# Optimization experiments

Measured on AMD Instinct MI355X. Metric: run time of the kernel, lower is better.

## Reference

```python
import jax, jax.numpy as jnp
import numpy as np
import math

H = 768      # hidden_size
NH = 12      # num_head
DH = H // NH # head dim
FF = 4 * H
EPS = 1e-6

def _layernorm(x, g, b):
    mu = jnp.mean(x, axis=-1, keepdims=True)
    var = jnp.mean(jnp.square(x - mu), axis=-1, keepdims=True)
    return (x - mu) * jax.lax.rsqrt(var + EPS) * g + b

def setup_inputs() -> dict:
    key = jax.random.key(0)
    ks = jax.random.split(key, 16)
    B, N = 8, 1024
    xav = lambda k, i, o: jax.random.uniform(k, (i, o), jnp.float32, -1.0, 1.0) * math.sqrt(6.0 / (i + o))
    bias = lambda k, o: jax.random.normal(k, (o,), jnp.float32) * 1e-6
    return {
        "x": jax.random.normal(ks[0], (B, N, H), jnp.float32),
        "wq": xav(ks[1], H, H), "bq": bias(ks[2], H),
        "wk": xav(ks[3], H, H), "bk": bias(ks[4], H),
        "wv": xav(ks[5], H, H), "bv": bias(ks[6], H),
        "wo": xav(ks[7], H, H), "bo": bias(ks[8], H),
        "w1": xav(ks[9], H, FF), "b1": bias(ks[10], FF),
        "w2": xav(ks[11], FF, H), "b2": bias(ks[12], H),
        "g1": jnp.ones((H,), jnp.float32), "be1": jnp.zeros((H,), jnp.float32),
        "g2": jnp.ones((H,), jnp.float32), "be2": jnp.zeros((H,), jnp.float32),
    }

def reference(x, wq, bq, wk, bk, wv, bv, wo, bo, w1, b1, w2, b2, g1, be1, g2, be2):
    B, N, _ = x.shape
    x1 = _layernorm(x, g1, be1)
    # QKV projections -> (B, NH, N, DH)
    split = lambda t: t.reshape(B, N, NH, DH).transpose(0, 2, 1, 3)
    q = split(x1 @ wq + bq)
    k = split(x1 @ wk + bk)
    v = split(x1 @ wv + bv)
    # NOTE: original divides by sqrt(attention_size)=sqrt(H), not sqrt(DH)
    scores = jnp.einsum("bhqd,bhkd->bhqk", q, k) / math.sqrt(H)
    weights = jax.nn.softmax(scores, axis=-1)
    ctx = jnp.einsum("bhqk,bhkd->bhqd", weights, v)
    ctx = ctx.transpose(0, 2, 1, 3).reshape(B, N, H)
    attn_out = ctx @ wo + bo  # dropout is identity in eval
    x = x + attn_out
    x2 = _layernorm(x, g2, be2)
    h = jax.nn.gelu(x2 @ w1 + b1, approximate=False)  # torch F.gelu is exact erf gelu
    mlp_out = h @ w2 + b2
    x = x + mlp_out
    return (x, weights)
```

## Files before the change

kernel.cpp:

```cpp
#include <hip/hip_runtime.h>
#include <cstdint>
#include <cstddef>

#define H 768
#define NHEAD 12
#define DH 64
#define FFD 3072
#define BATCH 8
#define SEQ 1024
#define NTOK (BATCH*SEQ)
#define QKVS 2304

typedef __bf16 bf16x8 __attribute__((ext_vector_type(8)));
typedef float  floatx4 __attribute__((ext_vector_type(4)));

#define MFMA_BF16(a,b,c) __builtin_amdgcn_mfma_f32_16x16x32_bf16((a),(b),(c),0,0,0)

__device__ __forceinline__ void gload16(const void* g, void* l) {
    __builtin_amdgcn_global_load_lds((const __attribute__((address_space(1))) void*)g,
                                     (__attribute__((address_space(3))) void*)l,
                                     16, 0, 0);
}

__global__ __launch_bounds__(256) void ln_kernel(const float* __restrict__ x,
                                                 const float* __restrict__ g,
                                                 const float* __restrict__ be,
                                                 __bf16* __restrict__ out) {
    int row  = blockIdx.x * 4 + (threadIdx.x >> 6);
    int lane = threadIdx.x & 63;
    const float* xr = x + (size_t)row * H;
    float v[12];
    float s = 0.f;
#pragma unroll
    for (int i = 0; i < 12; i++) { v[i] = xr[lane + i * 64]; s += v[i]; }
#pragma unroll
    for (int m = 32; m >= 1; m >>= 1) s += __shfl_xor(s, m, 64);
    float mu = s * (1.0f / H);
    float q = 0.f;
#pragma unroll
    for (int i = 0; i < 12; i++) { float d = v[i] - mu; q += d * d; }
#pragma unroll
    for (int m = 32; m >= 1; m >>= 1) q += __shfl_xor(q, m, 64);
    float rstd = rsqrtf(q * (1.0f / H) + 1e-6f);
    __bf16* orow = out + (size_t)row * H;
#pragma unroll
    for (int i = 0; i < 12; i++) {
        int c = lane + i * 64;
        orow[c] = (__bf16)((v[i] - mu) * rstd * g[c] + be[c]);
    }
}

__global__ __launch_bounds__(256) void wtrans_kernel(const float* __restrict__ W,
                                                     __bf16* __restrict__ T,
                                                     int K, int Nn) {
    __shared__ float tile[32][33];
    int tx = threadIdx.x & 31;
    int ty = threadIdx.x >> 5;
    int n0 = blockIdx.x * 32, k0 = blockIdx.y * 32;
#pragma unroll
    for (int i = 0; i < 32; i += 8)
        tile[ty + i][tx] = W[(size_t)(k0 + ty + i) * Nn + n0 + tx];
    __syncthreads();
#pragma unroll
    for (int i = 0; i < 32; i += 8)
        T[(size_t)(n0 + ty + i) * K + k0 + tx] = (__bf16)tile[tx][ty + i];
}

__global__ __launch_bounds__(256) void bcat_kernel(const float* __restrict__ bq,
                                                   const float* __restrict__ bk,
                                                   const float* __restrict__ bv,
                                                   float* __restrict__ o) {
    int i = blockIdx.x * 256 + threadIdx.x;
    if (i >= 3 * H) return;
    if (i < H) o[i] = bq[i];
    else if (i < 2 * H) o[i] = bk[i - H];
    else o[i] = bv[i - 2 * H];
}

__global__ __launch_bounds__(256) void vtrans_kernel(const __bf16* __restrict__ qkv,
                                                     __bf16* __restrict__ vT) {
    __shared__ __bf16 tile[64][65];
    int b = blockIdx.z, h = blockIdx.y, n0 = blockIdx.x * 64;
    int tx = threadIdx.x, ty = threadIdx.y;
#pragma unroll
    for (int r = ty; r < 64; r += 4)
        tile[r][tx] = qkv[((size_t)b * SEQ + n0 + r) * QKVS + 2 * H + h * DH + tx];
    __syncthreads();
#pragma unroll
    for (int c = ty; c < 64; c += 4)
        vT[(((size_t)b * NHEAD + h) * DH + c) * SEQ + n0 + tx] = tile[tx][c];
}

template<bool GELU, bool HAS_RES, bool OUT_BF16>
__global__ __launch_bounds__(256) void gemm_kernel(const __bf16* __restrict__ A,
                                                   const __bf16* __restrict__ Bt,
                                                   const float* __restrict__ bias,
                                                   const float* __restrict__ res,
                                                   __bf16* __restrict__ obf,
                                                   float* __restrict__ ofp,
                                                   int Nn, int K) {
    __shared__ __bf16 As[128 * 32];
    __shared__ __bf16 Bs[128 * 32];
    int tid = threadIdx.x;
    int wave = tid >> 6, lane = tid & 63;
    int wr = wave >> 1, wc = wave & 1;
    int l15 = lane & 15, quad = lane >> 4;

    floatx4 acc[4][4];
    floatx4 zero = {0.f, 0.f, 0.f, 0.f};
#pragma unroll
    for (int i = 0; i < 4; i++)
#pragma unroll
        for (int j = 0; j < 4; j++) acc[i][j] = zero;

    int c0 = wave * 2, c1 = c0 + 1;
    int lr = lane >> 2, lc = (lane & 3) * 8;
    const __bf16* Ag0 = A + (size_t)(blockIdx.y * 128 + c0 * 16 + lr) * K + lc;
    const __bf16* Ag1 = A + (size_t)(blockIdx.y * 128 + c1 * 16 + lr) * K + lc;
    const __bf16* Bg0 = Bt + (size_t)(blockIdx.x * 128 + c0 * 16 + lr) * K + lc;
    const __bf16* Bg1 = Bt + (size_t)(blockIdx.x * 128 + c1 * 16 + lr) * K + lc;
    __bf16* AsD0 = &As[c0 * 512];
    __bf16* AsD1 = &As[c1 * 512];
    __bf16* BsD0 = &Bs[c0 * 512];
    __bf16* BsD1 = &Bs[c1 * 512];

    for (int k0 = 0; k0 < K; k0 += 32) {
        gload16(Ag0 + k0, AsD0);
        gload16(Ag1 + k0, AsD1);
        gload16(Bg0 + k0, BsD0);
        gload16(Bg1 + k0, BsD1);
        __syncthreads();
        bf16x8 af[4], bfv[4];
#pragma unroll
        for (int i = 0; i < 4; i++)
            af[i] = *(const bf16x8*)&As[(wr * 64 + i * 16 + l15) * 32 + quad * 8];
#pragma unroll
        for (int j = 0; j < 4; j++)
            bfv[j] = *(const bf16x8*)&Bs[(wc * 64 + j * 16 + l15) * 32 + quad * 8];
#pragma unroll
        for (int i = 0; i < 4; i++)
#pragma unroll
            for (int j = 0; j < 4; j++)
                acc[i][j] = MFMA_BF16(af[i], bfv[j], acc[i][j]);
        __syncthreads();
    }

#pragma unroll
    for (int i = 0; i < 4; i++) {
        int row = blockIdx.y * 128 + wr * 64 + i * 16 + quad * 4;
#pragma unroll
        for (int j = 0; j < 4; j++) {
            int col = blockIdx.x * 128 + wc * 64 + j * 16 + l15;
            float bsv = bias[col];
#pragma unroll
            for (int r = 0; r < 4; r++) {
                float vv = acc[i][j][r] + bsv;
                if (GELU) vv = 0.5f * vv * (1.0f + erff(vv * 0.70710678118654752f));
                if (HAS_RES) vv += res[(size_t)(row + r) * Nn + col];
                if (OUT_BF16) obf[(size_t)(row + r) * Nn + col] = (__bf16)vv;
                else          ofp[(size_t)(row + r) * Nn + col] = vv;
            }
        }
    }
}

__device__ __forceinline__ int sbidx(int row, int col) {
    return row * 1024 + (col ^ ((row & 7) << 3));
}

__global__ __launch_bounds__(256, 4) void attn_kernel(const __bf16* __restrict__ qkv,
                                                      const __bf16* __restrict__ vT,
                                                      float* __restrict__ Wout,
                                                      __bf16* __restrict__ ctx) {
    __shared__ __bf16 Sb[16 * 1024];
    __shared__ __align__(16) float red[2][16][4];
    int tid = threadIdx.x;
    int wave = tid >> 6, lane = tid & 63, l15 = lane & 15, quad = lane >> 4;
    int rt = blockIdx.x, h = blockIdx.y, b = blockIdx.z;
    const size_t tokbase = (size_t)b * SEQ * QKVS + h * DH;
    const float scale = 0.03608439182435161f;

    const __bf16* qrow = qkv + tokbase + (size_t)(rt * 16 + l15) * QKVS;
    bf16x8 qf0 = *(const bf16x8*)(qrow + quad * 8);
    bf16x8 qf1 = *(const bf16x8*)(qrow + 32 + quad * 8);

    floatx4 s[16];
    const __bf16* kbase = qkv + tokbase + H;
#pragma unroll
    for (int i = 0; i < 16; i++) {
        int ct = wave * 16 + i;
        const __bf16* krow = kbase + (size_t)(ct * 16 + l15) * QKVS;
        bf16x8 kf0 = *(const bf16x8*)(krow + quad * 8);
        bf16x8 kf1 = *(const bf16x8*)(krow + 32 + quad * 8);
        floatx4 a = {0.f, 0.f, 0.f, 0.f};
        a = MFMA_BF16(qf0, kf0, a);
        a = MFMA_BF16(qf1, kf1, a);
#pragma unroll
        for (int r = 0; r < 4; r++) s[i][r] = a[r] * scale;
    }

    float m4[4];
#pragma unroll
    for (int r = 0; r < 4; r++) {
        float m = s[0][r];
#pragma unroll
        for (int i = 1; i < 16; i++) m = fmaxf(m, s[i][r]);
#pragma unroll
        for (int msk = 8; msk >= 1; msk >>= 1) m = fmaxf(m, __shfl_xor(m, msk, 64));
        m4[r] = m;
    }
    if (l15 == 0) {
#pragma unroll
        for (int r = 0; r < 4; r++) red[0][quad * 4 + r][wave] = m4[r];
    }
    __syncthreads();
    float mrow[4];
#pragma unroll
    for (int r = 0; r < 4; r++) {
        float4 rr = *(const float4*)&red[0][quad * 4 + r][0];
        mrow[r] = fmaxf(fmaxf(rr.x, rr.y), fmaxf(rr.z, rr.w));
    }

    float s4[4] = {0.f, 0.f, 0.f, 0.f};
#pragma unroll
    for (int i = 0; i < 16; i++) {
#pragma unroll
        for (int r = 0; r < 4; r++) {
            float e = __expf(s[i][r] - mrow[r]);
            s[i][r] = e;
            s4[r] += e;
        }
    }
#pragma unroll
    for (int r = 0; r < 4; r++) {
#pragma unroll
        for (int msk = 8; msk >= 1; msk >>= 1) s4[r] += __shfl_xor(s4[r], msk, 64);
    }
    if (l15 == 0) {
#pragma unroll
        for (int r = 0; r < 4; r++) red[1][quad * 4 + r][wave] = s4[r];
    }
    __syncthreads();
    float inv[4];
#pragma unroll
    for (int r = 0; r < 4; r++) {
        float4 rr = *(const float4*)&red[1][quad * 4 + r][0];
        inv[r] = 1.0f / (rr.x + rr.y + rr.z + rr.w);
    }

    size_t wbase = (((size_t)b * NHEAD + h) * SEQ + rt * 16) * SEQ;
#pragma unroll
    for (int i = 0; i < 16; i++) {
        int col = (wave * 16 + i) * 16 + l15;
#pragma unroll
        for (int r = 0; r < 4; r++) {
            float w = s[i][r] * inv[r];
            int row = quad * 4 + r;
            __builtin_nontemporal_store(w, &Wout[wbase + (size_t)row * SEQ + col]);
            Sb[sbidx(row, col)] = (__bf16)w;
        }
    }
    __syncthreads();

    floatx4 acc = {0.f, 0.f, 0.f, 0.f};
    const __bf16* vbase = vT + (((size_t)b * NHEAD + h) * DH + wave * 16 + l15) * SEQ;
#pragma unroll
    for (int c = 0; c < 32; c++) {
        int k0 = c * 32 + quad * 8;
        bf16x8 af = *(const bf16x8*)&Sb[sbidx(l15, k0)];
        bf16x8 bv = *(const bf16x8*)(vbase + k0);
        acc = MFMA_BF16(af, bv, acc);
    }
#pragma unroll
    for (int r = 0; r < 4; r++)
        ctx[((size_t)b * SEQ + rt * 16 + quad * 4 + r) * H + h * DH + wave * 16 + l15] =
            (__bf16)acc[r];
}

extern "C" void kernel_launch(void* const* d_in, const int* in_sizes, int n_in,
                              void* d_out, int out_size, void* d_ws, size_t ws_size,
                              hipStream_t stream) {
    const float* x   = (const float*)d_in[0];
    const float* wq  = (const float*)d_in[1];
    const float* bq  = (const float*)d_in[2];
    const float* wk  = (const float*)d_in[3];
    const float* bk  = (const float*)d_in[4];
    const float* wv  = (const float*)d_in[5];
    const float* bv  = (const float*)d_in[6];
    const float* wo  = (const float*)d_in[7];
    const float* bo  = (const float*)d_in[8];
    const float* w1  = (const float*)d_in[9];
    const float* b1  = (const float*)d_in[10];
    const float* w2  = (const float*)d_in[11];
    const float* b2  = (const float*)d_in[12];
    const float* g1  = (const float*)d_in[13];
    const float* be1 = (const float*)d_in[14];
    const float* g2  = (const float*)d_in[15];
    const float* be2 = (const float*)d_in[16];

    char* ws = (char*)d_ws;
    const size_t SZB = (size_t)NTOK * H * 2;
    __bf16* x1b  = (__bf16*)(ws);
    __bf16* qkvb = (__bf16*)(ws + SZB);
    __bf16* vTb  = (__bf16*)(ws + 4 * SZB);
    __bf16* ctxb = (__bf16*)(ws + 5 * SZB);
    __bf16* x2b  = (__bf16*)(ws + 6 * SZB);
    __bf16* hb   = (__bf16*)(ws + 7 * SZB);
    size_t off = 7 * SZB + (size_t)NTOK * FFD * 2;
    float* xattn = (float*)(ws + off); off += (size_t)NTOK * H * 4;
    __bf16* wqkvT = (__bf16*)(ws + off); off += (size_t)3 * H * H * 2;
    __bf16* woT  = (__bf16*)(ws + off); off += (size_t)H * H * 2;
    __bf16* w1T  = (__bf16*)(ws + off); off += (size_t)H * FFD * 2;
    __bf16* w2T  = (__bf16*)(ws + off); off += (size_t)FFD * H * 2;
    float* bqkv  = (float*)(ws + off); off += (size_t)3 * H * 4;

    float* outx = (float*)d_out;
    float* outw = (float*)d_out + (size_t)NTOK * H;

    wtrans_kernel<<<dim3(24, 24), 256, 0, stream>>>(wq, wqkvT, H, H);
    wtrans_kernel<<<dim3(24, 24), 256, 0, stream>>>(wk, wqkvT + (size_t)H * H, H, H);
    wtrans_kernel<<<dim3(24, 24), 256, 0, stream>>>(wv, wqkvT + (size_t)2 * H * H, H, H);
    wtrans_kernel<<<dim3(24, 24), 256, 0, stream>>>(wo, woT, H, H);
    wtrans_kernel<<<dim3(96, 24), 256, 0, stream>>>(w1, w1T, H, FFD);
    wtrans_kernel<<<dim3(24, 96), 256, 0, stream>>>(w2, w2T, FFD, H);
    bcat_kernel<<<9, 256, 0, stream>>>(bq, bk, bv, bqkv);

    ln_kernel<<<NTOK / 4, 256, 0, stream>>>(x, g1, be1, x1b);

    gemm_kernel<false, false, true><<<dim3(QKVS / 128, NTOK / 128), 256, 0, stream>>>(
        x1b, wqkvT, bqkv, nullptr, qkvb, nullptr, QKVS, H);

    vtrans_kernel<<<dim3(16, NHEAD, BATCH), dim3(64, 4), 0, stream>>>(qkvb, vTb);

    attn_kernel<<<dim3(64, NHEAD, BATCH), 256, 0, stream>>>(qkvb, vTb, outw, ctxb);

    gemm_kernel<false, true, false><<<dim3(H / 128, NTOK / 128), 256, 0, stream>>>(
        ctxb, woT, bo, x, nullptr, xattn, H, H);

    ln_kernel<<<NTOK / 4, 256, 0, stream>>>(xattn, g2, be2, x2b);

    gemm_kernel<true, false, true><<<dim3(FFD / 128, NTOK / 128), 256, 0, stream>>>(
        x2b, w1T, b1, nullptr, hb, nullptr, FFD, H);

    gemm_kernel<false, true, false><<<dim3(H / 128, NTOK / 128), 256, 0, stream>>>(
        hb, w2T, b2, xattn, nullptr, outx, H, FFD);
}
```

Before: 864.6 us.

## Merge prep kernels, use fast GELU erf approximation, remap attention blocks per XCD

Combines the six weight-transpose launches, the bias concat and the first layernorm into a single prep kernel, cutting seven kernel launches. Replaces erff in the GELU epilogue with an Abramowitz-Stegun polynomial built on a fast reciprocal and exponential, reducing epilogue ALU cost at some loss of accuracy. Remaps attention block indices so that all row tiles of a (batch, head) pair land on the same XCD, aiming to improve K/V reuse in that XCD's L2.

After: 851.3 us. No clear change (-1.5%).

```diff
diff --git a/kernel.cpp b/kernel.cpp
--- a/kernel.cpp
+++ b/kernel.cpp
@@ -20,6 +20,91 @@
     __builtin_amdgcn_global_load_lds((const __attribute__((address_space(1))) void*)g,
                                      (__attribute__((address_space(3))) void*)l,
                                      16, 0, 0);
+}
+
+__device__ __forceinline__ float gelu_erf(float x) {
+    float z = fabsf(x) * 0.70710678118654752f;
+    float t = __builtin_amdgcn_rcpf(1.0f + 0.3275911f * z);
+    float poly = t * (0.254829592f +
+               t * (-0.284496736f +
+               t * (1.421413741f +
+               t * (-1.453152027f +
+               t * 1.061405429f))));
+    float e = __expf(-z * z);
+    float erfv = 1.0f - poly * e;
+    erfv = copysignf(erfv, x);
+    return 0.5f * x * (1.0f + erfv);
+}
+
+__global__ __launch_bounds__(256) void prep_kernel(
+    const float* __restrict__ wq, const float* __restrict__ wk,
+    const float* __restrict__ wv, const float* __restrict__ wo,
+    const float* __restrict__ w1, const float* __restrict__ w2,
+    const float* __restrict__ bq, const float* __restrict__ bk,
+    const float* __restrict__ bv,
+    __bf16* __restrict__ wqkvT, __bf16* __restrict__ woT,
+    __bf16* __restrict__ w1T, __bf16* __restrict__ w2T,
+    float* __restrict__ bqkv,
+    const float* __restrict__ x, const float* __restrict__ g1,
+    const float* __restrict__ be1, __bf16* __restrict__ x1b) {
+    __shared__ float tile[32][33];
+    int bid = blockIdx.x;
+    int tid = threadIdx.x;
+    if (bid < 6912) {
+        const float* W; __bf16* T; int Kd, Nn, bx, by;
+        if (bid < 1728) {
+            int part = bid / 576;
+            int rem = bid - part * 576;
+            W = part == 0 ? wq : (part == 1 ? wk : wv);
+            T = wqkvT + (size_t)part * H * H;
+            Kd = H; Nn = H; bx = rem % 24; by = rem / 24;
+        } else if (bid < 2304) {
+            int rem = bid - 1728;
+            W = wo; T = woT; Kd = H; Nn = H; bx = rem % 24; by = rem / 24;
+        } else if (bid < 4608) {
+            int rem = bid - 2304;
+            W = w1; T = w1T; Kd = H; Nn = FFD; bx = rem % 96; by = rem / 96;
+        } else {
+            int rem = bid - 4608;
+            W = w2; T = w2T; Kd = FFD; Nn = H; bx = rem % 24; by = rem / 24;
+        }
+        int tx = tid & 31, ty = tid >> 5;
+        int n0 = bx * 32, k0 = by * 32;
+#pragma unroll
+        for (int i = 0; i < 32; i += 8)
+            tile[ty + i][tx] = W[(size_t)(k0 + ty + i) * Nn + n0 + tx];
+        __syncthreads();
+#pragma unroll
+        for (int i = 0; i < 32; i += 8)
+            T[(size_t)(n0 + ty + i) * Kd + k0 + tx] = (__bf16)tile[tx][ty + i];
+    } else if (bid < 6921) {
+        int i = (bid - 6912) * 256 + tid;
+        float v = i < H ? bq[i] : (i < 2 * H ? bk[i - H] : bv[i - 2 * H]);
+        bqkv[i] = v;
+    } else {
+        int row  = (bid - 6921) * 4 + (tid >> 6);
+        int lane = tid & 63;
+        const float* xr = x + (size_t)row * H;
+        float v[12];
+        float s = 0.f;
+#pragma unroll
+        for (int i = 0; i < 12; i++) { v[i] = xr[lane + i * 64]; s += v[i]; }
+#pragma unroll
+        for (int m = 32; m >= 1; m >>= 1) s += __shfl_xor(s, m, 64);
+        float mu = s * (1.0f / H);
+        float q = 0.f;
+#pragma unroll
+        for (int i = 0; i < 12; i++) { float d = v[i] - mu; q += d * d; }
+#pragma unroll
+        for (int m = 32; m >= 1; m >>= 1) q += __shfl_xor(q, m, 64);
+        float rstd = rsqrtf(q * (1.0f / H) + 1e-6f);
+        __bf16* orow = x1b + (size_t)row * H;
+#pragma unroll
+        for (int i = 0; i < 12; i++) {
+            int c = lane + i * 64;
+            orow[c] = (__bf16)((v[i] - mu) * rstd * g1[c] + be1[c]);
+        }
+    }
 }
 
 __global__ __launch_bounds__(256) void ln_kernel(const float* __restrict__ x,
@@ -48,33 +133,6 @@
         int c = lane + i * 64;
         orow[c] = (__bf16)((v[i] - mu) * rstd * g[c] + be[c]);
     }
-}
-
-__global__ __launch_bounds__(256) void wtrans_kernel(const float* __restrict__ W,
-                                                     __bf16* __restrict__ T,
-                                                     int K, int Nn) {
-    __shared__ float tile[32][33];
-    int tx = threadIdx.x & 31;
-    int ty = threadIdx.x >> 5;
-    int n0 = blockIdx.x * 32, k0 = blockIdx.y * 32;
-#pragma unroll
-    for (int i = 0; i < 32; i += 8)
-        tile[ty + i][tx] = W[(size_t)(k0 + ty + i) * Nn + n0 + tx];
-    __syncthreads();
-#pragma unroll
-    for (int i = 0; i < 32; i += 8)
-        T[(size_t)(n0 + ty + i) * K + k0 + tx] = (__bf16)tile[tx][ty + i];
-}
-
-__global__ __launch_bounds__(256) void bcat_kernel(const float* __restrict__ bq,
-                                                   const float* __restrict__ bk,
-                                                   const float* __restrict__ bv,
-                                                   float* __restrict__ o) {
-    int i = blockIdx.x * 256 + threadIdx.x;
-    if (i >= 3 * H) return;
-    if (i < H) o[i] = bq[i];
-    else if (i < 2 * H) o[i] = bk[i - H];
-    else o[i] = bv[i - 2 * H];
 }
 
 __global__ __launch_bounds__(256) void vtrans_kernel(const __bf16* __restrict__ qkv,
@@ -155,7 +213,7 @@
 #pragma unroll
             for (int r = 0; r < 4; r++) {
                 float vv = acc[i][j][r] + bsv;
-                if (GELU) vv = 0.5f * vv * (1.0f + erff(vv * 0.70710678118654752f));
+                if (GELU) vv = gelu_erf(vv);
                 if (HAS_RES) vv += res[(size_t)(row + r) * Nn + col];
                 if (OUT_BF16) obf[(size_t)(row + r) * Nn + col] = (__bf16)vv;
                 else          ofp[(size_t)(row + r) * Nn + col] = vv;
@@ -176,7 +234,14 @@
     __shared__ __align__(16) float red[2][16][4];
     int tid = threadIdx.x;
     int wave = tid >> 6, lane = tid & 63, l15 = lane & 15, quad = lane >> 4;
-    int rt = blockIdx.x, h = blockIdx.y, b = blockIdx.z;
+
+    int linear = blockIdx.x + 64 * (blockIdx.y + 12 * blockIdx.z);
+    int xcd = linear & 7;
+    int j   = linear >> 3;
+    int bh  = xcd + 8 * (j >> 6);
+    int rt  = j & 63;
+    int h = bh % NHEAD, b = bh / NHEAD;
+
     const size_t tokbase = (size_t)b * SEQ * QKVS + h * DH;
     const float scale = 0.03608439182435161f;
 
@@ -317,15 +382,9 @@
     float* outx = (float*)d_out;
     float* outw = (float*)d_out + (size_t)NTOK * H;
 
-    wtrans_kernel<<<dim3(24, 24), 256, 0, stream>>>(wq, wqkvT, H, H);
-    wtrans_kernel<<<dim3(24, 24), 256, 0, stream>>>(wk, wqkvT + (size_t)H * H, H, H);
-    wtrans_kernel<<<dim3(24, 24), 256, 0, stream>>>(wv, wqkvT + (size_t)2 * H * H, H, H);
-    wtrans_kernel<<<dim3(24, 24), 256, 0, stream>>>(wo, woT, H, H);
-    wtrans_kernel<<<dim3(96, 24), 256, 0, stream>>>(w1, w1T, H, FFD);
-    wtrans_kernel<<<dim3(24, 96), 256, 0, stream>>>(w2, w2T, FFD, H);
-    bcat_kernel<<<9, 256, 0, stream>>>(bq, bk, bv, bqkv);
-
-    ln_kernel<<<NTOK / 4, 256, 0, stream>>>(x, g1, be1, x1b);
+    prep_kernel<<<8969, 256, 0, stream>>>(wq, wk, wv, wo, w1, w2, bq, bk, bv,
+                                          wqkvT, woT, w1T, w2T, bqkv,
+                                          x, g1, be1, x1b);
 
     gemm_kernel<false, false, true><<<dim3(QKVS / 128, NTOK / 128), 256, 0, stream>>>(
         x1b, wqkvT, bqkv, nullptr, qkvb, nullptr, QKVS, H);
```
